# Performance work log

Hardware: AMD Instinct MI355X
Metric: run time of the kernel (lower is better)

The kernel has to match this reference:

```python
import jax, jax.numpy as jnp
import numpy as np

DIM = 512; HEADS = 8; KVH = 2; DH = 64; SEG = 1024; EPS = 1e-12
NA = 4096; NX = 4096; B = 2


def _mh_rmsnorm(t, gamma):
    # t: [b,h,n,d]; F.normalize (L2 with eps clamp) * gamma * sqrt(d)
    norm = jnp.maximum(jnp.linalg.norm(t, axis=-1, keepdims=True), EPS)
    return (t / norm) * gamma * (DH ** 0.5)


def _rope(t, pos):
    # rotate-half RoPE over full head dim
    half = DH // 2
    inv_freq = 1.0 / (10000.0 ** (jnp.arange(half, dtype=jnp.float32) / half))
    freqs = pos[:, None] * inv_freq[None, :]            # [n, half]
    cos = jnp.concatenate([jnp.cos(freqs)] * 2, -1)     # [n, d]
    sin = jnp.concatenate([jnp.sin(freqs)] * 2, -1)
    t1, t2 = jnp.split(t, 2, axis=-1)
    rot = jnp.concatenate([-t2, t1], -1)
    return t * cos + rot * sin


def _attend(q, k, v, beta):
    # infini-attention: per-segment causal softmax + kernelized recurrent memory
    b, h, n, d = q.shape
    pos = jnp.arange(n, dtype=jnp.float32)
    q = _rope(q, pos)
    k = _rope(k, pos)
    scale = d ** -0.5
    ns = n // SEG
    seg = lambda t: t.reshape(b, h, ns, SEG, d).transpose(2, 0, 1, 3, 4)
    qs, ks, vs = seg(q), seg(k), seg(v)                 # [ns,b,h,SEG,d]
    causal = jnp.tril(jnp.ones((SEG, SEG), dtype=bool))
    gate = jax.nn.sigmoid(beta)[None, :, None, None]    # [1,h,1,1]

    def step(carry, inp):
        M, z = carry                                    # [b,h,d,d], [b,h,d]
        qi, ki, vi = inp
        sq = jax.nn.elu(qi) + 1.0
        sk = jax.nn.elu(ki) + 1.0
        mem_num = jnp.einsum('bhnd,bhde->bhne', sq, M)
        mem_den = jnp.einsum('bhnd,bhd->bhn', sq, z)[..., None] + EPS
        a_mem = mem_num / mem_den
        scores = jnp.einsum('bhnd,bhmd->bhnm', qi, ki) * scale
        scores = jnp.where(causal, scores, -jnp.inf)
        a_loc = jnp.einsum('bhnm,bhmd->bhnd', jax.nn.softmax(scores, -1), vi)
        out = gate * a_mem + (1.0 - gate) * a_loc
        M = M + jnp.einsum('bhnd,bhne->bhde', sk, vi)
        z = z + sk.sum(axis=2)
        return (M, z), out

    M0 = jnp.zeros((b, h, d, d), q.dtype)
    z0 = jnp.zeros((b, h, d), q.dtype)
    _, outs = jax.lax.scan(step, (M0, z0), (qs, ks, vs))  # [ns,b,h,SEG,d]
    return outs.transpose(1, 2, 0, 3, 4).reshape(b, h, n, d)


def _heads(t, h):
    b, n, hd = t.shape
    return t.reshape(b, n, h, hd // h).transpose(0, 2, 1, 3)


def setup_inputs() -> dict:
    key = jax.random.key(0)
    ks = jax.random.split(key, 16)
    d = {}
    d['x'] = jax.random.normal(ks[0], (B, NX, DIM), jnp.float32)
    d['a'] = jax.random.normal(ks[1], (B, NA, DIM), jnp.float32)
    scale = 1.0 / np.sqrt(DIM)
    proj = [('Wq_x', HEADS * DH), ('Wk_x', KVH * DH), ('Wv_x', KVH * DH),
            ('Wq_a', HEADS * DH), ('Wk_a', KVH * DH), ('Wv_a', KVH * DH)]
    for i, (name, cout) in enumerate(proj):
        d[name] = jax.random.normal(ks[2 + i], (DIM, cout), jnp.float32) * scale
    d['gq_x'] = jnp.ones((HEADS, 1, DH), jnp.float32)
    d['gk_x'] = jnp.ones((KVH, 1, DH), jnp.float32)
    d['gq_a'] = jnp.ones((HEADS, 1, DH), jnp.float32)
    d['gk_a'] = jnp.ones((KVH, 1, DH), jnp.float32)
    d['beta'] = jnp.zeros((HEADS,), jnp.float32)
    return d


def reference(x, a, Wq_x, Wk_x, Wv_x, Wq_a, Wk_a, Wv_a, gq_x, gk_x, gq_a, gk_a, beta):
    rep = HEADS // KVH
    q_x = _mh_rmsnorm(_heads(x @ Wq_x, HEADS), gq_x)
    k_x = _mh_rmsnorm(_heads(x @ Wk_x, KVH), gk_x)
    v_x = _heads(x @ Wv_x, KVH)
    q_a = _mh_rmsnorm(_heads(a @ Wq_a, HEADS), gq_a)
    k_a = _mh_rmsnorm(_heads(a @ Wk_a, KVH), gk_a)
    v_a = _heads(a @ Wv_a, KVH)
    gqa = lambda t: jnp.tile(t, (1, rep, 1, 1))          # 'b h n d -> b (r h) n d'
    q = jnp.concatenate([q_a, q_x], axis=2)              # pack [a, x] along seq
    k = jnp.concatenate([gqa(k_a), gqa(k_x)], axis=2)
    v = jnp.concatenate([gqa(v_a), gqa(v_x)], axis=2)
    out = _attend(q, k, v, beta)
    out_a, out_x = out[:, :, :NA], out[:, :, NA:]
    merge = lambda t: t.transpose(0, 2, 1, 3).reshape(t.shape[0], t.shape[2], -1)
    return merge(out_x), merge(out_a)
```

## Files before the change

### kernel.cpp

```cpp
#include <hip/hip_runtime.h>
#include <math.h>

#define NH 8
#define NKV 2
#define SEGL 1024
#define NSEG 8
#define NTOK 8192
#define BATCH 2
#define DIMK 512

typedef short short8v __attribute__((ext_vector_type(8)));
typedef short short4v __attribute__((ext_vector_type(4)));
typedef float f32x4 __attribute__((ext_vector_type(4)));
typedef int int4v __attribute__((ext_vector_type(4)));

__device__ __forceinline__ unsigned short f2bf(float f) {
  union { float f; unsigned u; } c; c.f = f;
  unsigned u = c.u;
  return (unsigned short)((u + 0x7FFFu + ((u >> 16) & 1u)) >> 16);
}
__device__ __forceinline__ float bf2f(unsigned short h) {
  union { unsigned u; float f; } c; c.u = ((unsigned)h) << 16;
  return c.f;
}
__device__ __forceinline__ unsigned cvtpk(float lo, float hi) {
  unsigned r;
  asm("v_cvt_pk_bf16_f32 %0, %1, %2" : "=v"(r) : "v"(lo), "v"(hi));
  return r;
}

__device__ __forceinline__ void gload16(const unsigned short* g, unsigned short* l) {
  __builtin_amdgcn_global_load_lds(
      (const __attribute__((address_space(1))) unsigned int*)g,
      (__attribute__((address_space(3))) unsigned int*)l, 16, 0, 0);
}

__global__ void cast_bf16_kernel(const float* __restrict__ a, const float* __restrict__ x,
                                 unsigned short* __restrict__ outa,
                                 unsigned short* __restrict__ outx) {
  const float* in = blockIdx.y ? x : a;
  unsigned short* out = blockIdx.y ? outx : outa;
  int i = blockIdx.x * blockDim.x + threadIdx.x;
  const float4* p = (const float4*)in + (size_t)i * 2;
  float4 v0 = p[0], v1 = p[1];
  short8v o;
  o[0] = (short)f2bf(v0.x); o[1] = (short)f2bf(v0.y);
  o[2] = (short)f2bf(v0.z); o[3] = (short)f2bf(v0.w);
  o[4] = (short)f2bf(v1.x); o[5] = (short)f2bf(v1.y);
  o[6] = (short)f2bf(v1.z); o[7] = (short)f2bf(v1.w);
  *((short8v*)out + i) = o;
}

__global__ void rope_tab_kernel(float* __restrict__ tab) {
  const int i = blockIdx.x * 256 + threadIdx.x;
  const int pos = i >> 5, j = i & 31;
  const float LOG1E4 = 9.210340371976184f;
  float inv = __expf(-((float)j / 32.f) * LOG1E4);
  float sn, cs;
  sincosf((float)pos * inv, &sn, &cs);
  tab[(size_t)pos * 64 + j] = cs;
  tab[(size_t)pos * 64 + 32 + j] = sn;
}

__global__ void wtrans_kernel(const float* __restrict__ w0, const float* __restrict__ w1,
                              const float* __restrict__ w2, const float* __restrict__ w3,
                              const float* __restrict__ w4, const float* __restrict__ w5,
                              unsigned short* __restrict__ o0, unsigned short* __restrict__ o1,
                              unsigned short* __restrict__ o2, unsigned short* __restrict__ o3,
                              unsigned short* __restrict__ o4, unsigned short* __restrict__ o5) {
  __shared__ float T[32][33];
  const int z = blockIdx.z;
  const float* in; unsigned short* out; int C;
  switch (z) {
    case 0: in = w0; out = o0; C = 512; break;
    case 1: in = w1; out = o1; C = 128; break;
    case 2: in = w2; out = o2; C = 128; break;
    case 3: in = w3; out = o3; C = 512; break;
    case 4: in = w4; out = o4; C = 128; break;
    default: in = w5; out = o5; C = 128; break;
  }
  const int c0 = blockIdx.x * 32, k0 = blockIdx.y * 32;
  if (c0 >= C) return;
  const int tx = threadIdx.x & 31, ty = threadIdx.x >> 5;
  #pragma unroll
  for (int i = 0; i < 4; i++)
    T[ty + i * 8][tx] = in[(size_t)(k0 + ty + i * 8) * C + c0 + tx];
  __syncthreads();
  #pragma unroll
  for (int i = 0; i < 4; i++)
    out[(size_t)(c0 + ty + i * 8) * 512 + k0 + tx] = f2bf(T[tx][ty + i * 8]);
}

__global__ __launch_bounds__(256, 3) void proj_all_kernel(
    const unsigned short* __restrict__ Xa, const unsigned short* __restrict__ Xx,
    const unsigned short* __restrict__ WtQa, const unsigned short* __restrict__ WtKa,
    const unsigned short* __restrict__ WtVa, const unsigned short* __restrict__ WtQx,
    const unsigned short* __restrict__ WtKx, const unsigned short* __restrict__ WtVx,
    const float* __restrict__ gq_a, const float* __restrict__ gk_a,
    const float* __restrict__ gq_x, const float* __restrict__ gk_x,
    const float* __restrict__ Rtab,
    unsigned short* __restrict__ Qb, unsigned short* __restrict__ Kb,
    unsigned short* __restrict__ Kt, unsigned short* __restrict__ Vt)
{
  __shared__ __attribute__((aligned(16))) unsigned short Xs[2][128][64];
  __shared__ __attribute__((aligned(16))) unsigned short Ws2[2][64][64];
  unsigned short (*Tsh)[72] = (unsigned short (*)[72])&Xs[0][0][0];

  const int tid = threadIdx.x;
  const int w = tid >> 6, l = tid & 63, lc = l & 15, lg = l >> 4;
  const int r7 = lc & 7;
  const int z = blockIdx.z;
  const int y = blockIdx.y;
  const int row0 = blockIdx.x * 128;
  const int pos_offset = z ? 4096 : 0;

  const unsigned short* Xbf = z ? Xx : Xa;
  const unsigned short* Wt;
  const float* gamma = nullptr;
  unsigned short* OUT = nullptr;
  unsigned short* OUTT = nullptr;
  int h, Hout, doNR;
  if (y < 8) {
    h = y; Hout = NH; doNR = 1;
    Wt = z ? WtQx : WtQa; gamma = z ? gq_x : gq_a; OUT = Qb;
  } else if (y < 10) {
    h = y - 8; Hout = NKV; doNR = 1;
    Wt = z ? WtKx : WtKa; gamma = z ? gk_x : gk_a; OUT = Kb; OUTT = Kt;
  } else {
    h = y - 10; Hout = NKV; doNR = 0;
    Wt = z ? WtVx : WtVa; OUTT = Vt;
  }

  const int srow = tid >> 3;
  const int sg   = (tid & 7) ^ (srow & 7);
  const unsigned short* Xrow = Xbf + (size_t)(row0 + srow) * 512 + sg * 8;
  const unsigned short* Wrow = Wt + (size_t)(h * 64 + srow) * 512 + sg * 8;

  f32x4 acc[2][4];
  #pragma unroll
  for (int m = 0; m < 2; m++)
    #pragma unroll
    for (int ct = 0; ct < 4; ct++) { acc[m][ct][0]=0.f; acc[m][ct][1]=0.f; acc[m][ct][2]=0.f; acc[m][ct][3]=0.f; }

  #pragma unroll
  for (int p = 0; p < 4; p++)
    gload16(Xrow + (size_t)p * 32 * 512, &Xs[0][0][0] + p * 2048 + tid * 8);
  #pragma unroll
  for (int p = 0; p < 2; p++)
    gload16(Wrow + (size_t)p * 32 * 512, &Ws2[0][0][0] + p * 2048 + tid * 8);
  __syncthreads();

  for (int s = 0; s < 8; s++) {
    const int buf = s & 1;
    if (s < 7) {
      const int k0n = (s + 1) * 64;
      #pragma unroll
      for (int p = 0; p < 4; p++)
        gload16(Xrow + (size_t)p * 32 * 512 + k0n, &Xs[buf ^ 1][0][0] + p * 2048 + tid * 8);
      #pragma unroll
      for (int p = 0; p < 2; p++)
        gload16(Wrow + (size_t)p * 32 * 512 + k0n, &Ws2[buf ^ 1][0][0] + p * 2048 + tid * 8);
    }

    __builtin_amdgcn_s_setprio(1);
    #pragma unroll
    for (int kc = 0; kc < 2; kc++) {
      const int gsw = (((kc * 4 + lg) ^ r7) & 7) * 8;
      short8v a8[2], b8[4];
      #pragma unroll
      for (int m = 0; m < 2; m++)
        a8[m] = *(const short8v*)&Xs[buf][m * 64 + w * 16 + lc][gsw];
      #pragma unroll
      for (int ct = 0; ct < 4; ct++)
        b8[ct] = *(const short8v*)&Ws2[buf][ct * 16 + lc][gsw];
      #pragma unroll
      for (int m = 0; m < 2; m++)
        #pragma unroll
        for (int ct = 0; ct < 4; ct++)
          acc[m][ct] = __builtin_amdgcn_mfma_f32_16x16x32_bf16(a8[m], b8[ct], acc[m][ct], 0, 0, 0);
    }
    __builtin_amdgcn_s_setprio(0);
    __syncthreads();
  }

  float gam[4];
  if (doNR) {
    #pragma unroll
    for (int ct = 0; ct < 4; ct++) gam[ct] = gamma[h * 64 + ct * 16 + lc];
  }

  #pragma unroll
  for (int m = 0; m < 2; m++) {
    if (doNR) {
      float srw[4];
      #pragma unroll
      for (int reg = 0; reg < 4; reg++) {
        float ss = acc[m][0][reg]*acc[m][0][reg] + acc[m][1][reg]*acc[m][1][reg]
                 + acc[m][2][reg]*acc[m][2][reg] + acc[m][3][reg]*acc[m][3][reg];
        ss += __shfl_xor(ss, 1, 64);
        ss += __shfl_xor(ss, 2, 64);
        ss += __shfl_xor(ss, 4, 64);
        ss += __shfl_xor(ss, 8, 64);
        srw[reg] = 8.0f / fmaxf(sqrtf(ss), 1e-12f);
      }
      const int posb = pos_offset + ((row0 + m * 64) & 4095) + w * 16 + lg * 4;
      #pragma unroll
      for (int reg = 0; reg < 4; reg++) {
        const float* tabr = Rtab + (size_t)(posb + reg) * 64;
        #pragma unroll
        for (int half = 0; half < 2; half++) {
          float cs = tabr[half * 16 + lc];
          float sn = tabr[32 + half * 16 + lc];
          float v1 = acc[m][half][reg] * srw[reg] * gam[half];
          float v2 = acc[m][half + 2][reg] * srw[reg] * gam[half + 2];
          acc[m][half][reg]     = v1 * cs - v2 * sn;
          acc[m][half + 2][reg] = v2 * cs + v1 * sn;
        }
      }
    }

    #pragma unroll
    for (int ct = 0; ct < 4; ct++)
      #pragma unroll
      for (int reg = 0; reg < 4; reg++)
        Tsh[w * 16 + lg * 4 + reg][ct * 16 + lc] = f2bf(acc[m][ct][reg]);
    __syncthreads();

    const int growm = row0 + m * 64;
    const int b = growm >> 12;
    const int pos0 = pos_offset + (growm & 4095);
    if (OUT) {
      const int r = tid >> 2, part = tid & 3;
      unsigned short* dst = OUT + (((size_t)b * Hout + h) * NTOK + pos0 + r) * 64 + part * 16;
      short8v u0 = *(const short8v*)&Tsh[r][part * 16];
      short8v u1 = *(const short8v*)&Tsh[r][part * 16 + 8];
      *(short8v*)dst = u0;
      *(short8v*)(dst + 8) = u1;
    }
    if (OUTT) {
      const int e = tid >> 2, part = tid & 3;
      short8v t0, t1;
      #pragma unroll
      for (int jj = 0; jj < 16; jj++) {
        const int LG = ((part & 1) << 1) | (jj >> 3);
        const int H  = (jj >> 2) & 1;
        const int I  = jj & 3;
        const int srcrow = (part >> 1) * 32 + H * 16 + LG * 4 + I;
        unsigned short v = Tsh[srcrow][e];
        if (jj < 8) t0[jj] = (short)v; else t1[jj - 8] = (short)v;
      }
      unsigned short* dstT = OUTT + (((size_t)b * NKV + h) * 64 + e) * NTOK + pos0 + part * 16;
      *(short8v*)dstT = t0;
      *(short8v*)(dstT + 8) = t1;
    }
    __syncthreads();
  }
}

__global__ __launch_bounds__(256) void seg_summary_kernel(
    const unsigned short* __restrict__ Kt, const unsigned short* __restrict__ Vt,
    float* __restrict__ Spart, float* __restrict__ Zpart)
{
  const int blk = blockIdx.x;
  const int chunk = blk & 7;
  const int seg = (blk >> 3) & 7;
  const int bkv = blk >> 6;
  const int tid = threadIdx.x;
  const int w = tid >> 6, l = tid & 63, lc = l & 15, lg = l >> 4;
  const unsigned short* KtB = Kt + ((size_t)bkv * 64) * NTOK + seg * SEGL + chunk * 128;
  const unsigned short* VtB = Vt + ((size_t)bkv * 64) * NTOK + seg * SEGL + chunk * 128;

  f32x4 acc[4];
  #pragma unroll
  for (int ct = 0; ct < 4; ct++) { acc[ct][0]=0.f; acc[ct][1]=0.f; acc[ct][2]=0.f; acc[ct][3]=0.f; }
  float zacc[4] = {0.f, 0.f, 0.f, 0.f};

  for (int n0 = 0; n0 < 128; n0 += 32) {
    short8v av = *(const short8v*)(VtB + (size_t)(w * 16 + lc) * NTOK + n0 + lg * 8);
    #pragma unroll
    for (int ct = 0; ct < 4; ct++) {
      short8v kv = *(const short8v*)(KtB + (size_t)(ct * 16 + lc) * NTOK + n0 + lg * 8);
      short8v skv;
      float zp = 0.f;
      #pragma unroll
      for (int i = 0; i < 8; i++) {
        float kf = bf2f((unsigned short)kv[i]);
        float sk = kf > 0.f ? kf + 1.f : __expf(kf);
        zp += sk;
        skv[i] = (short)f2bf(sk);
      }
      zacc[ct] += zp;
      acc[ct] = __builtin_amdgcn_mfma_f32_16x16x32_bf16(av, skv, acc[ct], 0, 0, 0);
    }
  }

  float* Sp = Spart + (size_t)blk * 4096;
  #pragma unroll
  for (int ct = 0; ct < 4; ct++)
    #pragma unroll
    for (int reg = 0; reg < 4; reg++)
      Sp[(size_t)(w * 16 + lg * 4 + reg) * 64 + ct * 16 + lc] = acc[ct][reg];

  if (w == 0) {
    #pragma unroll
    for (int ct = 0; ct < 4; ct++) {
      zacc[ct] += __shfl_xor(zacc[ct], 16, 64);
      zacc[ct] += __shfl_xor(zacc[ct], 32, 64);
    }
    if (lg == 0) {
      float* Zp = Zpart + (size_t)blk * 64;
      #pragma unroll
      for (int ct = 0; ct < 4; ct++) Zp[ct * 16 + lc] = zacc[ct];
    }
  }
}

__global__ void prefix_kernel(const float* __restrict__ Spart, const float* __restrict__ Zpart,
                              unsigned short* __restrict__ PT, float* __restrict__ PZ)
{
  const int bkv = blockIdx.x;
  const int col = blockIdx.y * 256 + threadIdx.x;
  float run = 0.f;
  for (int s = 0; s < NSEG; s++) {
    float v = 0.f;
    #pragma unroll
    for (int c = 0; c < 8; c++)
      v += Spart[(((size_t)(bkv * 8 + s)) * 8 + c) * 4096 + col];
    PT[((size_t)bkv * 8 + s) * 4096 + col] = f2bf(run);
    run += v;
  }
  if (blockIdx.y == 0 && threadIdx.x < 64) {
    const int d = threadIdx.x;
    float rz = 0.f;
    for (int s = 0; s < NSEG; s++) {
      float v = 0.f;
      #pragma unroll
      for (int c = 0; c < 8; c++)
        v += Zpart[(((size_t)(bkv * 8 + s)) * 8 + c) * 64 + d];
      PZ[((size_t)bkv * 8 + s) * 64 + d] = rz;
      rz += v;
    }
  }
}

__global__ __launch_bounds__(256, 2) void attn_mfma_kernel(
    const unsigned short* __restrict__ Qb, const unsigned short* __restrict__ Kb,
    const unsigned short* __restrict__ Vt, const unsigned short* __restrict__ PT,
    const float* __restrict__ PZ, const float* __restrict__ beta,
    float* __restrict__ OUT)
{
  __shared__ __attribute__((aligned(16))) unsigned short Ks[2][64][64];
  __shared__ __attribute__((aligned(16))) unsigned short Vs[2][64][64];
  const int tid = threadIdx.x;
  const int w = tid >> 6;
  const int l = tid & 63;
  const int lc = l & 15;
  const int lg = l >> 4;
  const int r7 = lc & 7;

  const int bid = (blockIdx.x & 7) * 64 + (blockIdx.x >> 3);
  const int j   = bid & 7;
  const int seg = (bid >> 3) & 7;
  const int pp  = (bid >> 6) & 1;
  const int kv  = (bid >> 7) & 1;
  const int b   = bid >> 8;
  const int bkv = b * NKV + kv;
  const int qtA = 15 - j, qtB = j;
  const int segbase = seg * SEGL;

  const unsigned short* Kbase = Kb + ((size_t)bkv * NTOK + segbase) * 64;
  const unsigned short* Vbase = Vt + ((size_t)bkv * 64) * NTOK + segbase;

  const int srow = tid >> 3;
  const int sg   = (tid & 7) ^ (srow & 7);

  short8v aq0[2][2], aq1[2][2];
  #pragma unroll
  for (int hh = 0; hh < 2; hh++) {
    const int h = kv + 4 * pp + 2 * hh;
    const int bh = b * NH + h;
    {
      const unsigned short* qp =
          Qb + (((size_t)bh * NTOK) + segbase + qtA * 64 + w * 16 + lc) * 64 + lg * 8;
      aq0[hh][0] = *(const short8v*)(qp);
      aq1[hh][0] = *(const short8v*)(qp + 32);
    }
    {
      const unsigned short* qp =
          Qb + (((size_t)bh * NTOK) + segbase + qtB * 64 + w * 16 + lc) * 64 + lg * 8;
      aq0[hh][1] = *(const short8v*)(qp);
      aq1[hh][1] = *(const short8v*)(qp + 32);
    }
  }

  f32x4 O[2][2][4];
  #pragma unroll
  for (int hh = 0; hh < 2; hh++)
    #pragma unroll
    for (int tt = 0; tt < 2; tt++)
      #pragma unroll
      for (int ce = 0; ce < 4; ce++) { O[hh][tt][ce][0]=0.f; O[hh][tt][ce][1]=0.f; O[hh][tt][ce][2]=0.f; O[hh][tt][ce][3]=0.f; }
  float rsumL[2][2] = {{0.f, 0.f}, {0.f, 0.f}};

  const float c1 = 0.125f * 1.44269504089f;
  const float c2 = 8.0f * 1.44269504089f;

  {
    unsigned short* kD = &Ks[0][0][0];
    unsigned short* vD = &Vs[0][0][0];
    #pragma unroll
    for (int p = 0; p < 2; p++) {
      const int row = p * 32 + srow;
      gload16(Kbase + (size_t)row * 64 + sg * 8, kD + p * 2048 + tid * 8);
      gload16(Vbase + (size_t)row * NTOK + sg * 8, vD + p * 2048 + tid * 8);
    }
  }
  __syncthreads();

  for (int kt = 0; kt <= qtA; ++kt) {
    const int buf = kt & 1;
    if (kt < qtA) {
      const int ktn = kt + 1;
      unsigned short* kD = &Ks[buf ^ 1][0][0];
      unsigned short* vD = &Vs[buf ^ 1][0][0];
      #pragma unroll
      for (int p = 0; p < 2; p++) {
        const int row = p * 32 + srow;
        gload16(Kbase + (size_t)(ktn * 64 + row) * 64 + sg * 8, kD + p * 2048 + tid * 8);
        gload16(Vbase + (size_t)row * NTOK + ktn * 64 + sg * 8, vD + p * 2048 + tid * 8);
      }
    }

    __builtin_amdgcn_s_setprio(1);

    short8v ak0r[4], ak1r[4];
    #pragma unroll
    for (int ck = 0; ck < 4; ck++) {
      const int krow = ck * 16 + lc;
      ak0r[ck] = *(const short8v*)&Ks[buf][krow][((lg ^ r7) & 7) * 8];
      ak1r[ck] = *(const short8v*)&Ks[buf][krow][(((lg + 4) ^ r7) & 7) * 8];
    }
    short8v bvr[2][4];
    #pragma unroll
    for (int cp = 0; cp < 2; cp++)
      #pragma unroll
      for (int ce = 0; ce < 4; ce++)
        bvr[cp][ce] = *(const short8v*)&Vs[buf][ce * 16 + lc][(((cp * 4 + lg) ^ r7) & 7) * 8];

    #pragma unroll
    for (int hh = 0; hh < 2; hh++) {
      #pragma unroll
      for (int tt = 0; tt < 2; tt++) {
        if (tt == 1 && kt > qtB) continue;
        const int qt_ = tt ? qtB : qtA;
        const bool diag = (kt == qt_);
        const int ctmax = diag ? w : 3;

        unsigned paw[4][2];
        #pragma unroll
        for (int ck = 0; ck < 4; ck++) {
          if (ck > ctmax) { paw[ck][0] = 0u; paw[ck][1] = 0u; continue; }
          f32x4 s;
          s[0]=0.f; s[1]=0.f; s[2]=0.f; s[3]=0.f;
          s = __builtin_amdgcn_mfma_f32_16x16x32_bf16(ak0r[ck], aq0[hh][tt], s, 0, 0, 0);
          s = __builtin_amdgcn_mfma_f32_16x16x32_bf16(ak1r[ck], aq1[hh][tt], s, 0, 0, 0);
          const bool needmask = diag && (ck == w);
          float p0 = exp2f(s[0] * c1 - c2);
          float p1 = exp2f(s[1] * c1 - c2);
          float p2 = exp2f(s[2] * c1 - c2);
          float p3 = exp2f(s[3] * c1 - c2);
          if (needmask) {
            if (lg * 4 + 0 > lc) p0 = 0.f;
            if (lg * 4 + 1 > lc) p1 = 0.f;
            if (lg * 4 + 2 > lc) p2 = 0.f;
            if (lg * 4 + 3 > lc) p3 = 0.f;
          }
          rsumL[hh][tt] += p0 + p1 + p2 + p3;
          paw[ck][0] = cvtpk(p0, p1);
          paw[ck][1] = cvtpk(p2, p3);
        }

        #pragma unroll
        for (int cp = 0; cp < 2; cp++) {
          if (cp * 2 > ctmax) continue;
          int4v a8i;
          a8i[0] = (int)paw[cp * 2][0];
          a8i[1] = (int)paw[cp * 2][1];
          a8i[2] = (int)paw[cp * 2 + 1][0];
          a8i[3] = (int)paw[cp * 2 + 1][1];
          short8v a8;
          __builtin_memcpy(&a8, &a8i, 16);
          #pragma unroll
          for (int ce = 0; ce < 4; ce++)
            O[hh][tt][ce] = __builtin_amdgcn_mfma_f32_16x16x32_bf16(a8, bvr[cp][ce], O[hh][tt][ce], 0, 0, 0);
        }
      }
    }
    __builtin_amdgcn_s_setprio(0);
    __syncthreads();
  }

  const unsigned short* stp = PT + ((size_t)bkv * NSEG + seg) * 4096 + lc * 64 + lg * 8;
  const float* zp = PZ + ((size_t)bkv * NSEG + seg) * 64 + lg * 8;

  #pragma unroll
  for (int hh = 0; hh < 2; hh++) {
    const int h = kv + 4 * pp + 2 * hh;
    const float g = 1.f / (1.f + __expf(-beta[h]));
    const float g1 = 1.f - g;

    #pragma unroll
    for (int tt = 0; tt < 2; tt++) {
      float rsum = rsumL[hh][tt];
      rsum += __shfl_xor(rsum, 16, 64);
      rsum += __shfl_xor(rsum, 32, 64);

      float sq0[8], sq1[8];
      float den = 1e-12f;
      #pragma unroll
      for (int i = 0; i < 8; i++) {
        float f0 = bf2f((unsigned short)aq0[hh][tt][i]);
        sq0[i] = f0 > 0.f ? f0 + 1.f : __expf(f0);
        den += sq0[i] * zp[i];
        float f1 = bf2f((unsigned short)aq1[hh][tt][i]);
        sq1[i] = f1 > 0.f ? f1 + 1.f : __expf(f1);
        den += sq1[i] * zp[32 + i];
      }
      int4v q0i, q1i;
      q0i[0] = (int)cvtpk(sq0[0], sq0[1]);
      q0i[1] = (int)cvtpk(sq0[2], sq0[3]);
      q0i[2] = (int)cvtpk(sq0[4], sq0[5]);
      q0i[3] = (int)cvtpk(sq0[6], sq0[7]);
      q1i[0] = (int)cvtpk(sq1[0], sq1[1]);
      q1i[1] = (int)cvtpk(sq1[2], sq1[3]);
      q1i[2] = (int)cvtpk(sq1[4], sq1[5]);
      q1i[3] = (int)cvtpk(sq1[6], sq1[7]);
      short8v asq0, asq1;
      __builtin_memcpy(&asq0, &q0i, 16);
      __builtin_memcpy(&asq1, &q1i, 16);

      f32x4 N[4];
      #pragma unroll
      for (int ct = 0; ct < 4; ct++) { N[ct][0]=0.f; N[ct][1]=0.f; N[ct][2]=0.f; N[ct][3]=0.f; }
      #pragma unroll
      for (int ct = 0; ct < 4; ct++) {
        short8v bs0 = *(const short8v*)(stp + ct * 16 * 64);
        short8v bs1 = *(const short8v*)(stp + ct * 16 * 64 + 32);
        N[ct] = __builtin_amdgcn_mfma_f32_16x16x32_bf16(asq0, bs0, N[ct], 0, 0, 0);
        N[ct] = __builtin_amdgcn_mfma_f32_16x16x32_bf16(asq1, bs1, N[ct], 0, 0, 0);
      }
      den += __shfl_xor(den, 16, 64);
      den += __shfl_xor(den, 32, 64);
      float denc[4], rs[4];
      #pragma unroll
      for (int reg = 0; reg < 4; reg++) {
        denc[reg] = __shfl(den, lg * 4 + reg, 64);
        rs[reg]   = __shfl(rsum, lg * 4 + reg, 64);
      }

      const int q0 = (tt ? qtB : qtA) * 64;
      const int nrow = segbase + q0 + w * 16 + lg * 4;
      #pragma unroll
      for (int reg = 0; reg < 4; reg++) {
        const int n = nrow + reg;
        const float invs = 1.f / rs[reg];
        const float invd = 1.f / denc[reg];
        size_t obase;
        if (n < 4096) obase = (size_t)BATCH * 4096 * 512 + (((size_t)b * 4096 + n) * NH + h) * 64;
        else          obase = (((size_t)b * 4096 + (n - 4096)) * NH + h) * 64;
        #pragma unroll
        for (int ce = 0; ce < 4; ce++) {
          OUT[obase + ce * 16 + lc] = g * N[ce][reg] * invd + g1 * O[hh][tt][ce][reg] * invs;
        }
      }
    }
  }
}

extern "C" void kernel_launch(void* const* d_in, const int* in_sizes, int n_in,
                              void* d_out, int out_size, void* d_ws, size_t ws_size,
                              hipStream_t stream) {
  const float* x    = (const float*)d_in[0];
  const float* a    = (const float*)d_in[1];
  const float* Wq_x = (const float*)d_in[2];
  const float* Wk_x = (const float*)d_in[3];
  const float* Wv_x = (const float*)d_in[4];
  const float* Wq_a = (const float*)d_in[5];
  const float* Wk_a = (const float*)d_in[6];
  const float* Wv_a = (const float*)d_in[7];
  const float* gq_x = (const float*)d_in[8];
  const float* gk_x = (const float*)d_in[9];
  const float* gq_a = (const float*)d_in[10];
  const float* gk_a = (const float*)d_in[11];
  const float* beta = (const float*)d_in[12];

  unsigned short* Qb = (unsigned short*)d_ws;
  unsigned short* Kb = Qb + (size_t)8388608;
  unsigned short* Kt = Kb + (size_t)2097152;
  unsigned short* Vt = Kt + (size_t)2097152;
  unsigned short* Xa = Vt + (size_t)2097152;
  unsigned short* Xx = Xa + (size_t)4194304;
  unsigned short* WtQa = Xx + (size_t)4194304;
  unsigned short* WtKa = WtQa + (size_t)262144;
  unsigned short* WtVa = WtKa + (size_t)65536;
  unsigned short* WtQx = WtVa + (size_t)65536;
  unsigned short* WtKx = WtQx + (size_t)262144;
  unsigned short* WtVx = WtKx + (size_t)65536;
  float* Spart = (float*)(WtVx + (size_t)65536);
  float* Zpart = Spart + (size_t)1048576;
  float* PZ = Zpart + (size_t)16384;
  unsigned short* PT = (unsigned short*)(PZ + (size_t)2048);
  float* Rtab = (float*)(PT + (size_t)131072);

  cast_bf16_kernel<<<dim3(2048, 2), 256, 0, stream>>>(a, x, Xa, Xx);
  rope_tab_kernel<<<1024, 256, 0, stream>>>(Rtab);
  wtrans_kernel<<<dim3(16, 16, 6), 256, 0, stream>>>(
      Wq_a, Wk_a, Wv_a, Wq_x, Wk_x, Wv_x, WtQa, WtKa, WtVa, WtQx, WtKx, WtVx);
  proj_all_kernel<<<dim3(64, 12, 2), 256, 0, stream>>>(
      Xa, Xx, WtQa, WtKa, WtVa, WtQx, WtKx, WtVx,
      gq_a, gk_a, gq_x, gk_x, Rtab, Qb, Kb, Kt, Vt);
  seg_summary_kernel<<<256, 256, 0, stream>>>(Kt, Vt, Spart, Zpart);
  prefix_kernel<<<dim3(4, 16), 256, 0, stream>>>(Spart, Zpart, PT, PZ);
  attn_mfma_kernel<<<dim3(512), 256, 0, stream>>>(Qb, Kb, Vt, PT, PZ, beta, (float*)d_out);
}
```

Before: 93.80 us.

## Split attention blocks to one head each and fuse rope table into wtrans

The attention kernel now processes one query head per block instead of two, doubling the grid to 1024 blocks and raising the launch-bounds occupancy hint from 2 to 4 blocks per CU. This cuts per-thread registers and adds parallelism, at the cost of loading each K/V tile into shared memory twice as often. Separately, the RoPE table computation is folded into the weight-transpose kernel as an extra z-slice, removing one kernel launch.

```diff
diff --git a/kernel.cpp b/kernel.cpp
--- a/kernel.cpp
+++ b/kernel.cpp
@@ -51,25 +51,30 @@
   *((short8v*)out + i) = o;
 }
 
-__global__ void rope_tab_kernel(float* __restrict__ tab) {
-  const int i = blockIdx.x * 256 + threadIdx.x;
-  const int pos = i >> 5, j = i & 31;
-  const float LOG1E4 = 9.210340371976184f;
-  float inv = __expf(-((float)j / 32.f) * LOG1E4);
-  float sn, cs;
-  sincosf((float)pos * inv, &sn, &cs);
-  tab[(size_t)pos * 64 + j] = cs;
-  tab[(size_t)pos * 64 + 32 + j] = sn;
-}
-
 __global__ void wtrans_kernel(const float* __restrict__ w0, const float* __restrict__ w1,
                               const float* __restrict__ w2, const float* __restrict__ w3,
                               const float* __restrict__ w4, const float* __restrict__ w5,
                               unsigned short* __restrict__ o0, unsigned short* __restrict__ o1,
                               unsigned short* __restrict__ o2, unsigned short* __restrict__ o3,
-                              unsigned short* __restrict__ o4, unsigned short* __restrict__ o5) {
+                              unsigned short* __restrict__ o4, unsigned short* __restrict__ o5,
+                              float* __restrict__ rtab) {
   __shared__ float T[32][33];
   const int z = blockIdx.z;
+  if (z == 6) {
+    const int flat = blockIdx.y * 16 + blockIdx.x;
+    const int base = (flat * 256 + threadIdx.x) * 8;
+    const float LOG1E4 = 9.210340371976184f;
+    #pragma unroll
+    for (int k = 0; k < 8; k++) {
+      int e = base + k;
+      int pos = e >> 6, c = e & 63, jj = c & 31;
+      float inv = __expf(-((float)jj / 32.f) * LOG1E4);
+      float sn, cs;
+      sincosf((float)pos * inv, &sn, &cs);
+      rtab[e] = (c < 32) ? cs : sn;
+    }
+    return;
+  }
   const float* in; unsigned short* out; int C;
   switch (z) {
     case 0: in = w0; out = o0; C = 512; break;
@@ -343,7 +348,7 @@
   }
 }
 
-__global__ __launch_bounds__(256, 2) void attn_mfma_kernel(
+__global__ __launch_bounds__(256, 4) void attn_mfma_kernel(
     const unsigned short* __restrict__ Qb, const unsigned short* __restrict__ Kb,
     const unsigned short* __restrict__ Vt, const unsigned short* __restrict__ PT,
     const float* __restrict__ PZ, const float* __restrict__ beta,
@@ -358,12 +363,14 @@
   const int lg = l >> 4;
   const int r7 = lc & 7;
 
-  const int bid = (blockIdx.x & 7) * 64 + (blockIdx.x >> 3);
+  const int bid = (blockIdx.x & 7) * 128 + (blockIdx.x >> 3);
   const int j   = bid & 7;
   const int seg = (bid >> 3) & 7;
-  const int pp  = (bid >> 6) & 1;
-  const int kv  = (bid >> 7) & 1;
-  const int b   = bid >> 8;
+  const int hi  = (bid >> 6) & 3;
+  const int kv  = (bid >> 8) & 1;
+  const int b   = bid >> 9;
+  const int h   = kv + 2 * hi;
+  const int bh  = b * NH + h;
   const int bkv = b * NKV + kv;
   const int qtA = 15 - j, qtB = j;
   const int segbase = seg * SEGL;
@@ -374,33 +381,26 @@
   const int srow = tid >> 3;
   const int sg   = (tid & 7) ^ (srow & 7);
 
-  short8v aq0[2][2], aq1[2][2];
-  #pragma unroll
-  for (int hh = 0; hh < 2; hh++) {
-    const int h = kv + 4 * pp + 2 * hh;
-    const int bh = b * NH + h;
-    {
-      const unsigned short* qp =
-          Qb + (((size_t)bh * NTOK) + segbase + qtA * 64 + w * 16 + lc) * 64 + lg * 8;
-      aq0[hh][0] = *(const short8v*)(qp);
-      aq1[hh][0] = *(const short8v*)(qp + 32);
-    }
-    {
-      const unsigned short* qp =
-          Qb + (((size_t)bh * NTOK) + segbase + qtB * 64 + w * 16 + lc) * 64 + lg * 8;
-      aq0[hh][1] = *(const short8v*)(qp);
-      aq1[hh][1] = *(const short8v*)(qp + 32);
-    }
-  }
-
-  f32x4 O[2][2][4];
-  #pragma unroll
-  for (int hh = 0; hh < 2; hh++)
-    #pragma unroll
-    for (int tt = 0; tt < 2; tt++)
-      #pragma unroll
-      for (int ce = 0; ce < 4; ce++) { O[hh][tt][ce][0]=0.f; O[hh][tt][ce][1]=0.f; O[hh][tt][ce][2]=0.f; O[hh][tt][ce][3]=0.f; }
-  float rsumL[2][2] = {{0.f, 0.f}, {0.f, 0.f}};
+  short8v aq0[2], aq1[2];
+  {
+    const unsigned short* qp =
+        Qb + (((size_t)bh * NTOK) + segbase + qtA * 64 + w * 16 + lc) * 64 + lg * 8;
+    aq0[0] = *(const short8v*)(qp);
+    aq1[0] = *(const short8v*)(qp + 32);
+  }
+  {
+    const unsigned short* qp =
+        Qb + (((size_t)bh * NTOK) + segbase + qtB * 64 + w * 16 + lc) * 64 + lg * 8;
+    aq0[1] = *(const short8v*)(qp);
+    aq1[1] = *(const short8v*)(qp + 32);
+  }
+
+  f32x4 O[2][4];
+  #pragma unroll
+  for (int tt = 0; tt < 2; tt++)
+    #pragma unroll
+    for (int ce = 0; ce < 4; ce++) { O[tt][ce][0]=0.f; O[tt][ce][1]=0.f; O[tt][ce][2]=0.f; O[tt][ce][3]=0.f; }
+  float rsumL[2] = {0.f, 0.f};
 
   const float c1 = 0.125f * 1.44269504089f;
   const float c2 = 8.0f * 1.44269504089f;
@@ -448,52 +448,49 @@
         bvr[cp][ce] = *(const short8v*)&Vs[buf][ce * 16 + lc][(((cp * 4 + lg) ^ r7) & 7) * 8];
 
     #pragma unroll
-    for (int hh = 0; hh < 2; hh++) {
-      #pragma unroll
-      for (int tt = 0; tt < 2; tt++) {
-        if (tt == 1 && kt > qtB) continue;
-        const int qt_ = tt ? qtB : qtA;
-        const bool diag = (kt == qt_);
-        const int ctmax = diag ? w : 3;
-
-        unsigned paw[4][2];
+    for (int tt = 0; tt < 2; tt++) {
+      if (tt == 1 && kt > qtB) continue;
+      const int qt_ = tt ? qtB : qtA;
+      const bool diag = (kt == qt_);
+      const int ctmax = diag ? w : 3;
+
+      unsigned paw[4][2];
+      #pragma unroll
+      for (int ck = 0; ck < 4; ck++) {
+        if (ck > ctmax) { paw[ck][0] = 0u; paw[ck][1] = 0u; continue; }
+        f32x4 s;
+        s[0]=0.f; s[1]=0.f; s[2]=0.f; s[3]=0.f;
+        s = __builtin_amdgcn_mfma_f32_16x16x32_bf16(ak0r[ck], aq0[tt], s, 0, 0, 0);
+        s = __builtin_amdgcn_mfma_f32_16x16x32_bf16(ak1r[ck], aq1[tt], s, 0, 0, 0);
+        const bool needmask = diag && (ck == w);
+        float p0 = exp2f(s[0] * c1 - c2);
+        float p1 = exp2f(s[1] * c1 - c2);
+        float p2 = exp2f(s[2] * c1 - c2);
+        float p3 = exp2f(s[3] * c1 - c2);
+        if (needmask) {
+          if (lg * 4 + 0 > lc) p0 = 0.f;
+          if (lg * 4 + 1 > lc) p1 = 0.f;
+          if (lg * 4 + 2 > lc) p2 = 0.f;
+          if (lg * 4 + 3 > lc) p3 = 0.f;
+        }
+        rsumL[tt] += p0 + p1 + p2 + p3;
+        paw[ck][0] = cvtpk(p0, p1);
+        paw[ck][1] = cvtpk(p2, p3);
+      }
+
+      #pragma unroll
+      for (int cp = 0; cp < 2; cp++) {
+        if (cp * 2 > ctmax) continue;
+        int4v a8i;
+        a8i[0] = (int)paw[cp * 2][0];
+        a8i[1] = (int)paw[cp * 2][1];
+        a8i[2] = (int)paw[cp * 2 + 1][0];
+        a8i[3] = (int)paw[cp * 2 + 1][1];
+        short8v a8;
+        __builtin_memcpy(&a8, &a8i, 16);
         #pragma unroll
-        for (int ck = 0; ck < 4; ck++) {
-          if (ck > ctmax) { paw[ck][0] = 0u; paw[ck][1] = 0u; continue; }
-          f32x4 s;
-          s[0]=0.f; s[1]=0.f; s[2]=0.f; s[3]=0.f;
-          s = __builtin_amdgcn_mfma_f32_16x16x32_bf16(ak0r[ck], aq0[hh][tt], s, 0, 0, 0);
-          s = __builtin_amdgcn_mfma_f32_16x16x32_bf16(ak1r[ck], aq1[hh][tt], s, 0, 0, 0);
-          const bool needmask = diag && (ck == w);
-          float p0 = exp2f(s[0] * c1 - c2);
-          float p1 = exp2f(s[1] * c1 - c2);
-          float p2 = exp2f(s[2] * c1 - c2);
-          float p3 = exp2f(s[3] * c1 - c2);
-          if (needmask) {
-            if (lg * 4 + 0 > lc) p0 = 0.f;
-            if (lg * 4 + 1 > lc) p1 = 0.f;
-            if (lg * 4 + 2 > lc) p2 = 0.f;
-            if (lg * 4 + 3 > lc) p3 = 0.f;
-          }
-          rsumL[hh][tt] += p0 + p1 + p2 + p3;
-          paw[ck][0] = cvtpk(p0, p1);
-          paw[ck][1] = cvtpk(p2, p3);
-        }
-
-        #pragma unroll
-        for (int cp = 0; cp < 2; cp++) {
-          if (cp * 2 > ctmax) continue;
-          int4v a8i;
-          a8i[0] = (int)paw[cp * 2][0];
-          a8i[1] = (int)paw[cp * 2][1];
-          a8i[2] = (int)paw[cp * 2 + 1][0];
-          a8i[3] = (int)paw[cp * 2 + 1][1];
-          short8v a8;
-          __builtin_memcpy(&a8, &a8i, 16);
-          #pragma unroll
-          for (int ce = 0; ce < 4; ce++)
-            O[hh][tt][ce] = __builtin_amdgcn_mfma_f32_16x16x32_bf16(a8, bvr[cp][ce], O[hh][tt][ce], 0, 0, 0);
-        }
+        for (int ce = 0; ce < 4; ce++)
+          O[tt][ce] = __builtin_amdgcn_mfma_f32_16x16x32_bf16(a8, bvr[cp][ce], O[tt][ce], 0, 0, 0);
       }
     }
     __builtin_amdgcn_s_setprio(0);
@@ -502,76 +499,71 @@
 
   const unsigned short* stp = PT + ((size_t)bkv * NSEG + seg) * 4096 + lc * 64 + lg * 8;
   const float* zp = PZ + ((size_t)bkv * NSEG + seg) * 64 + lg * 8;
-
-  #pragma unroll
-  for (int hh = 0; hh < 2; hh++) {
-    const int h = kv + 4 * pp + 2 * hh;
-    const float g = 1.f / (1.f + __expf(-beta[h]));
-    const float g1 = 1.f - g;
-
-    #pragma unroll
-    for (int tt = 0; tt < 2; tt++) {
-      float rsum = rsumL[hh][tt];
-      rsum += __shfl_xor(rsum, 16, 64);
-      rsum += __shfl_xor(rsum, 32, 64);
-
-      float sq0[8], sq1[8];
-      float den = 1e-12f;
-      #pragma unroll
-      for (int i = 0; i < 8; i++) {
-        float f0 = bf2f((unsigned short)aq0[hh][tt][i]);
-        sq0[i] = f0 > 0.f ? f0 + 1.f : __expf(f0);
-        den += sq0[i] * zp[i];
-        float f1 = bf2f((unsigned short)aq1[hh][tt][i]);
-        sq1[i] = f1 > 0.f ? f1 + 1.f : __expf(f1);
-        den += sq1[i] * zp[32 + i];
-      }
-      int4v q0i, q1i;
-      q0i[0] = (int)cvtpk(sq0[0], sq0[1]);
-      q0i[1] = (int)cvtpk(sq0[2], sq0[3]);
-      q0i[2] = (int)cvtpk(sq0[4], sq0[5]);
-      q0i[3] = (int)cvtpk(sq0[6], sq0[7]);
-      q1i[0] = (int)cvtpk(sq1[0], sq1[1]);
-      q1i[1] = (int)cvtpk(sq1[2], sq1[3]);
-      q1i[2] = (int)cvtpk(sq1[4], sq1[5]);
-      q1i[3] = (int)cvtpk(sq1[6], sq1[7]);
-      short8v asq0, asq1;
-      __builtin_memcpy(&asq0, &q0i, 16);
-      __builtin_memcpy(&asq1, &q1i, 16);
-
-      f32x4 N[4];
-      #pragma unroll
-      for (int ct = 0; ct < 4; ct++) { N[ct][0]=0.f; N[ct][1]=0.f; N[ct][2]=0.f; N[ct][3]=0.f; }
-      #pragma unroll
-      for (int ct = 0; ct < 4; ct++) {
-        short8v bs0 = *(const short8v*)(stp + ct * 16 * 64);
-        short8v bs1 = *(const short8v*)(stp + ct * 16 * 64 + 32);
-        N[ct] = __builtin_amdgcn_mfma_f32_16x16x32_bf16(asq0, bs0, N[ct], 0, 0, 0);
-        N[ct] = __builtin_amdgcn_mfma_f32_16x16x32_bf16(asq1, bs1, N[ct], 0, 0, 0);
-      }
-      den += __shfl_xor(den, 16, 64);
-      den += __shfl_xor(den, 32, 64);
-      float denc[4], rs[4];
-      #pragma unroll
-      for (int reg = 0; reg < 4; reg++) {
-        denc[reg] = __shfl(den, lg * 4 + reg, 64);
-        rs[reg]   = __shfl(rsum, lg * 4 + reg, 64);
-      }
-
-      const int q0 = (tt ? qtB : qtA) * 64;
-      const int nrow = segbase + q0 + w * 16 + lg * 4;
-      #pragma unroll
-      for (int reg = 0; reg < 4; reg++) {
-        const int n = nrow + reg;
-        const float invs = 1.f / rs[reg];
-        const float invd = 1.f / denc[reg];
-        size_t obase;
-        if (n < 4096) obase = (size_t)BATCH * 4096 * 512 + (((size_t)b * 4096 + n) * NH + h) * 64;
-        else          obase = (((size_t)b * 4096 + (n - 4096)) * NH + h) * 64;
-        #pragma unroll
-        for (int ce = 0; ce < 4; ce++) {
-          OUT[obase + ce * 16 + lc] = g * N[ce][reg] * invd + g1 * O[hh][tt][ce][reg] * invs;
-        }
+  const float g = 1.f / (1.f + __expf(-beta[h]));
+  const float g1 = 1.f - g;
+
+  #pragma unroll
+  for (int tt = 0; tt < 2; tt++) {
+    float rsum = rsumL[tt];
+    rsum += __shfl_xor(rsum, 16, 64);
+    rsum += __shfl_xor(rsum, 32, 64);
+
+    float sq0[8], sq1[8];
+    float den = 1e-12f;
+    #pragma unroll
+    for (int i = 0; i < 8; i++) {
+      float f0 = bf2f((unsigned short)aq0[tt][i]);
+      sq0[i] = f0 > 0.f ? f0 + 1.f : __expf(f0);
+      den += sq0[i] * zp[i];
+      float f1 = bf2f((unsigned short)aq1[tt][i]);
+      sq1[i] = f1 > 0.f ? f1 + 1.f : __expf(f1);
+      den += sq1[i] * zp[32 + i];
+    }
+    int4v q0i, q1i;
+    q0i[0] = (int)cvtpk(sq0[0], sq0[1]);
+    q0i[1] = (int)cvtpk(sq0[2], sq0[3]);
+    q0i[2] = (int)cvtpk(sq0[4], sq0[5]);
+    q0i[3] = (int)cvtpk(sq0[6], sq0[7]);
+    q1i[0] = (int)cvtpk(sq1[0], sq1[1]);
+    q1i[1] = (int)cvtpk(sq1[2], sq1[3]);
+    q1i[2] = (int)cvtpk(sq1[4], sq1[5]);
+    q1i[3] = (int)cvtpk(sq1[6], sq1[7]);
+    short8v asq0, asq1;
+    __builtin_memcpy(&asq0, &q0i, 16);
+    __builtin_memcpy(&asq1, &q1i, 16);
+
+    f32x4 N[4];
+    #pragma unroll
+    for (int ct = 0; ct < 4; ct++) { N[ct][0]=0.f; N[ct][1]=0.f; N[ct][2]=0.f; N[ct][3]=0.f; }
+    #pragma unroll
+    for (int ct = 0; ct < 4; ct++) {
+      short8v bs0 = *(const short8v*)(stp + ct * 16 * 64);
+      short8v bs1 = *(const short8v*)(stp + ct * 16 * 64 + 32);
+      N[ct] = __builtin_amdgcn_mfma_f32_16x16x32_bf16(asq0, bs0, N[ct], 0, 0, 0);
+      N[ct] = __builtin_amdgcn_mfma_f32_16x16x32_bf16(asq1, bs1, N[ct], 0, 0, 0);
+    }
+    den += __shfl_xor(den, 16, 64);
+    den += __shfl_xor(den, 32, 64);
+    float denc[4], rs[4];
+    #pragma unroll
+    for (int reg = 0; reg < 4; reg++) {
+      denc[reg] = __shfl(den, lg * 4 + reg, 64);
+      rs[reg]   = __shfl(rsum, lg * 4 + reg, 64);
+    }
+
+    const int q0 = (tt ? qtB : qtA) * 64;
+    const int nrow = segbase + q0 + w * 16 + lg * 4;
+    #pragma unroll
+    for (int reg = 0; reg < 4; reg++) {
+      const int n = nrow + reg;
+      const float invs = 1.f / rs[reg];
+      const float invd = 1.f / denc[reg];
+      size_t obase;
+      if (n < 4096) obase = (size_t)BATCH * 4096 * 512 + (((size_t)b * 4096 + n) * NH + h) * 64;
+      else          obase = (((size_t)b * 4096 + (n - 4096)) * NH + h) * 64;
+      #pragma unroll
+      for (int ce = 0; ce < 4; ce++) {
+        OUT[obase + ce * 16 + lc] = g * N[ce][reg] * invd + g1 * O[tt][ce][reg] * invs;
       }
     }
   }
@@ -613,13 +605,12 @@
   float* Rtab = (float*)(PT + (size_t)131072);
 
   cast_bf16_kernel<<<dim3(2048, 2), 256, 0, stream>>>(a, x, Xa, Xx);
-  rope_tab_kernel<<<1024, 256, 0, stream>>>(Rtab);
-  wtrans_kernel<<<dim3(16, 16, 6), 256, 0, stream>>>(
-      Wq_a, Wk_a, Wv_a, Wq_x, Wk_x, Wv_x, WtQa, WtKa, WtVa, WtQx, WtKx, WtVx);
+  wtrans_kernel<<<dim3(16, 16, 7), 256, 0, stream>>>(
+      Wq_a, Wk_a, Wv_a, Wq_x, Wk_x, Wv_x, WtQa, WtKa, WtVa, WtQx, WtKx, WtVx, Rtab);
   proj_all_kernel<<<dim3(64, 12, 2), 256, 0, stream>>>(
       Xa, Xx, WtQa, WtKa, WtVa, WtQx, WtKx, WtVx,
       gq_a, gk_a, gq_x, gk_x, Rtab, Qb, Kb, Kt, Vt);
   seg_summary_kernel<<<256, 256, 0, stream>>>(Kt, Vt, Spart, Zpart);
   prefix_kernel<<<dim3(4, 16), 256, 0, stream>>>(Spart, Zpart, PT, PZ);
-  attn_mfma_kernel<<<dim3(512), 256, 0, stream>>>(Qb, Kb, Vt, PT, PZ, beta, (float*)d_out);
-}
+  attn_mfma_kernel<<<dim3(1024), 256, 0, stream>>>(Qb, Kb, Vt, PT, PZ, beta, (float*)d_out);
+}
```

After: 150.5 us. +60.4%, slower.

## Stage two KV tiles per barrier in attention and fold rope table into wtrans

Applied to the files above, without the earlier changes.

The attention kernel moves from a 2-deep to a 4-deep LDS ring and processes two key/value tiles between each barrier, prefetching the next two tiles while computing. This halves the number of __syncthreads per block and gives loads more time to land. Separately, the RoPE table generation is merged into the weight-transpose launch as an extra z-slice, which removes one kernel launch. LDS use per block doubles, which could limit occupancy at two blocks per CU, and the code size grows from duplicating the tile compute.

```diff
diff --git a/kernel.cpp b/kernel.cpp
--- a/kernel.cpp
+++ b/kernel.cpp
@@ -13,6 +13,8 @@
 typedef short short4v __attribute__((ext_vector_type(4)));
 typedef float f32x4 __attribute__((ext_vector_type(4)));
 typedef int int4v __attribute__((ext_vector_type(4)));
+
+#define MFMA16 __builtin_amdgcn_mfma_f32_16x16x32_bf16
 
 __device__ __forceinline__ unsigned short f2bf(float f) {
   union { float f; unsigned u; } c; c.f = f;
@@ -51,25 +53,30 @@
   *((short8v*)out + i) = o;
 }
 
-__global__ void rope_tab_kernel(float* __restrict__ tab) {
-  const int i = blockIdx.x * 256 + threadIdx.x;
-  const int pos = i >> 5, j = i & 31;
-  const float LOG1E4 = 9.210340371976184f;
-  float inv = __expf(-((float)j / 32.f) * LOG1E4);
-  float sn, cs;
-  sincosf((float)pos * inv, &sn, &cs);
-  tab[(size_t)pos * 64 + j] = cs;
-  tab[(size_t)pos * 64 + 32 + j] = sn;
-}
-
 __global__ void wtrans_kernel(const float* __restrict__ w0, const float* __restrict__ w1,
                               const float* __restrict__ w2, const float* __restrict__ w3,
                               const float* __restrict__ w4, const float* __restrict__ w5,
                               unsigned short* __restrict__ o0, unsigned short* __restrict__ o1,
                               unsigned short* __restrict__ o2, unsigned short* __restrict__ o3,
-                              unsigned short* __restrict__ o4, unsigned short* __restrict__ o5) {
+                              unsigned short* __restrict__ o4, unsigned short* __restrict__ o5,
+                              float* __restrict__ rtab) {
   __shared__ float T[32][33];
   const int z = blockIdx.z;
+  if (z == 6) {
+    const int flat = blockIdx.y * 16 + blockIdx.x;
+    const int base = (flat * 256 + threadIdx.x) * 8;
+    const float LOG1E4 = 9.210340371976184f;
+    #pragma unroll
+    for (int k = 0; k < 8; k++) {
+      int e = base + k;
+      int pos = e >> 6, c = e & 63, jj = c & 31;
+      float inv = __expf(-((float)jj / 32.f) * LOG1E4);
+      float sn, cs;
+      sincosf((float)pos * inv, &sn, &cs);
+      rtab[e] = (c < 32) ? cs : sn;
+    }
+    return;
+  }
   const float* in; unsigned short* out; int C;
   switch (z) {
     case 0: in = w0; out = o0; C = 512; break;
@@ -177,7 +184,7 @@
       for (int m = 0; m < 2; m++)
         #pragma unroll
         for (int ct = 0; ct < 4; ct++)
-          acc[m][ct] = __builtin_amdgcn_mfma_f32_16x16x32_bf16(a8[m], b8[ct], acc[m][ct], 0, 0, 0);
+          acc[m][ct] = MFMA16(a8[m], b8[ct], acc[m][ct], 0, 0, 0);
     }
     __builtin_amdgcn_s_setprio(0);
     __syncthreads();
@@ -290,7 +297,7 @@
         skv[i] = (short)f2bf(sk);
       }
       zacc[ct] += zp;
-      acc[ct] = __builtin_amdgcn_mfma_f32_16x16x32_bf16(av, skv, acc[ct], 0, 0, 0);
+      acc[ct] = MFMA16(av, skv, acc[ct], 0, 0, 0);
     }
   }
 
@@ -343,14 +350,95 @@
   }
 }
 
+#define STAGE_TILE(TILE, BUFN)                                                 \
+  do {                                                                         \
+    unsigned short* kD_ = &Ks[BUFN][0][0];                                     \
+    unsigned short* vD_ = &Vs[BUFN][0][0];                                     \
+    _Pragma("unroll")                                                          \
+    for (int p_ = 0; p_ < 2; p_++) {                                           \
+      const int row_ = p_ * 32 + srow;                                         \
+      gload16(Kbase + (size_t)((TILE) * 64 + row_) * 64 + sg * 8,              \
+              kD_ + p_ * 2048 + tid * 8);                                      \
+      gload16(Vbase + (size_t)row_ * NTOK + (TILE) * 64 + sg * 8,              \
+              vD_ + p_ * 2048 + tid * 8);                                      \
+    }                                                                          \
+  } while (0)
+
+#define COMPUTE_KT(KT)                                                         \
+  do {                                                                         \
+    const int kt_ = (KT);                                                      \
+    const int buf_ = kt_ & 3;                                                  \
+    short8v ak0r[4], ak1r[4];                                                  \
+    _Pragma("unroll")                                                          \
+    for (int ck = 0; ck < 4; ck++) {                                           \
+      const int krow = ck * 16 + lc;                                           \
+      ak0r[ck] = *(const short8v*)&Ks[buf_][krow][((lg ^ r7) & 7) * 8];        \
+      ak1r[ck] = *(const short8v*)&Ks[buf_][krow][(((lg + 4) ^ r7) & 7) * 8];  \
+    }                                                                          \
+    short8v bvr[2][4];                                                         \
+    _Pragma("unroll")                                                          \
+    for (int cp = 0; cp < 2; cp++)                                             \
+      _Pragma("unroll")                                                        \
+      for (int ce = 0; ce < 4; ce++)                                           \
+        bvr[cp][ce] =                                                          \
+            *(const short8v*)&Vs[buf_][ce * 16 + lc][(((cp * 4 + lg) ^ r7) & 7) * 8]; \
+    _Pragma("unroll")                                                          \
+    for (int hh = 0; hh < 2; hh++) {                                           \
+      _Pragma("unroll")                                                        \
+      for (int tt = 0; tt < 2; tt++) {                                         \
+        if (tt == 1 && kt_ > qtB) continue;                                    \
+        const int qt_ = tt ? qtB : qtA;                                        \
+        const bool diag = (kt_ == qt_);                                        \
+        const int ctmax = diag ? w : 3;                                        \
+        unsigned paw[4][2];                                                    \
+        _Pragma("unroll")                                                      \
+        for (int ck = 0; ck < 4; ck++) {                                       \
+          if (ck > ctmax) { paw[ck][0] = 0u; paw[ck][1] = 0u; continue; }      \
+          f32x4 s;                                                             \
+          s[0] = 0.f; s[1] = 0.f; s[2] = 0.f; s[3] = 0.f;                      \
+          s = MFMA16(ak0r[ck], aq0[hh][tt], s, 0, 0, 0);                       \
+          s = MFMA16(ak1r[ck], aq1[hh][tt], s, 0, 0, 0);                       \
+          const bool needmask = diag && (ck == w);                             \
+          float p0 = exp2f(s[0] * c1 - c2);                                    \
+          float p1 = exp2f(s[1] * c1 - c2);                                    \
+          float p2 = exp2f(s[2] * c1 - c2);                                    \
+          float p3 = exp2f(s[3] * c1 - c2);                                    \
+          if (needmask) {                                                      \
+            if (lg * 4 + 0 > lc) p0 = 0.f;                                     \
+            if (lg * 4 + 1 > lc) p1 = 0.f;                                     \
+            if (lg * 4 + 2 > lc) p2 = 0.f;                                     \
+            if (lg * 4 + 3 > lc) p3 = 0.f;                                     \
+          }                                                                    \
+          rsumL[hh][tt] += p0 + p1 + p2 + p3;                                  \
+          paw[ck][0] = cvtpk(p0, p1);                                          \
+          paw[ck][1] = cvtpk(p2, p3);                                          \
+        }                                                                      \
+        _Pragma("unroll")                                                      \
+        for (int cp = 0; cp < 2; cp++) {                                       \
+          if (cp * 2 > ctmax) continue;                                        \
+          int4v a8i;                                                           \
+          a8i[0] = (int)paw[cp * 2][0];                                        \
+          a8i[1] = (int)paw[cp * 2][1];                                        \
+          a8i[2] = (int)paw[cp * 2 + 1][0];                                    \
+          a8i[3] = (int)paw[cp * 2 + 1][1];                                    \
+          short8v a8;                                                          \
+          __builtin_memcpy(&a8, &a8i, 16);                                     \
+          _Pragma("unroll")                                                    \
+          for (int ce = 0; ce < 4; ce++)                                       \
+            O[hh][tt][ce] = MFMA16(a8, bvr[cp][ce], O[hh][tt][ce], 0, 0, 0);   \
+        }                                                                      \
+      }                                                                        \
+    }                                                                          \
+  } while (0)
+
 __global__ __launch_bounds__(256, 2) void attn_mfma_kernel(
     const unsigned short* __restrict__ Qb, const unsigned short* __restrict__ Kb,
     const unsigned short* __restrict__ Vt, const unsigned short* __restrict__ PT,
     const float* __restrict__ PZ, const float* __restrict__ beta,
     float* __restrict__ OUT)
 {
-  __shared__ __attribute__((aligned(16))) unsigned short Ks[2][64][64];
-  __shared__ __attribute__((aligned(16))) unsigned short Vs[2][64][64];
+  __shared__ __attribute__((aligned(16))) unsigned short Ks[4][64][64];
+  __shared__ __attribute__((aligned(16))) unsigned short Vs[4][64][64];
   const int tid = threadIdx.x;
   const int w = tid >> 6;
   const int l = tid & 63;
@@ -405,97 +493,17 @@
   const float c1 = 0.125f * 1.44269504089f;
   const float c2 = 8.0f * 1.44269504089f;
 
-  {
-    unsigned short* kD = &Ks[0][0][0];
-    unsigned short* vD = &Vs[0][0][0];
-    #pragma unroll
-    for (int p = 0; p < 2; p++) {
-      const int row = p * 32 + srow;
-      gload16(Kbase + (size_t)row * 64 + sg * 8, kD + p * 2048 + tid * 8);
-      gload16(Vbase + (size_t)row * NTOK + sg * 8, vD + p * 2048 + tid * 8);
-    }
-  }
+  STAGE_TILE(0, 0);
+  STAGE_TILE(1, 1);
   __syncthreads();
 
-  for (int kt = 0; kt <= qtA; ++kt) {
-    const int buf = kt & 1;
-    if (kt < qtA) {
-      const int ktn = kt + 1;
-      unsigned short* kD = &Ks[buf ^ 1][0][0];
-      unsigned short* vD = &Vs[buf ^ 1][0][0];
-      #pragma unroll
-      for (int p = 0; p < 2; p++) {
-        const int row = p * 32 + srow;
-        gload16(Kbase + (size_t)(ktn * 64 + row) * 64 + sg * 8, kD + p * 2048 + tid * 8);
-        gload16(Vbase + (size_t)row * NTOK + ktn * 64 + sg * 8, vD + p * 2048 + tid * 8);
-      }
-    }
+  for (int kt0 = 0; kt0 <= qtA; kt0 += 2) {
+    if (kt0 + 2 <= qtA) STAGE_TILE(kt0 + 2, (kt0 + 2) & 3);
+    if (kt0 + 3 <= qtA) STAGE_TILE(kt0 + 3, (kt0 + 3) & 3);
 
     __builtin_amdgcn_s_setprio(1);
-
-    short8v ak0r[4], ak1r[4];
-    #pragma unroll
-    for (int ck = 0; ck < 4; ck++) {
-      const int krow = ck * 16 + lc;
-      ak0r[ck] = *(const short8v*)&Ks[buf][krow][((lg ^ r7) & 7) * 8];
-      ak1r[ck] = *(const short8v*)&Ks[buf][krow][(((lg + 4) ^ r7) & 7) * 8];
-    }
-    short8v bvr[2][4];
-    #pragma unroll
-    for (int cp = 0; cp < 2; cp++)
-      #pragma unroll
-      for (int ce = 0; ce < 4; ce++)
-        bvr[cp][ce] = *(const short8v*)&Vs[buf][ce * 16 + lc][(((cp * 4 + lg) ^ r7) & 7) * 8];
-
-    #pragma unroll
-    for (int hh = 0; hh < 2; hh++) {
-      #pragma unroll
-      for (int tt = 0; tt < 2; tt++) {
-        if (tt == 1 && kt > qtB) continue;
-        const int qt_ = tt ? qtB : qtA;
-        const bool diag = (kt == qt_);
-        const int ctmax = diag ? w : 3;
-
-        unsigned paw[4][2];
-        #pragma unroll
-        for (int ck = 0; ck < 4; ck++) {
-          if (ck > ctmax) { paw[ck][0] = 0u; paw[ck][1] = 0u; continue; }
-          f32x4 s;
-          s[0]=0.f; s[1]=0.f; s[2]=0.f; s[3]=0.f;
-          s = __builtin_amdgcn_mfma_f32_16x16x32_bf16(ak0r[ck], aq0[hh][tt], s, 0, 0, 0);
-          s = __builtin_amdgcn_mfma_f32_16x16x32_bf16(ak1r[ck], aq1[hh][tt], s, 0, 0, 0);
-          const bool needmask = diag && (ck == w);
-          float p0 = exp2f(s[0] * c1 - c2);
-          float p1 = exp2f(s[1] * c1 - c2);
-          float p2 = exp2f(s[2] * c1 - c2);
-          float p3 = exp2f(s[3] * c1 - c2);
-          if (needmask) {
-            if (lg * 4 + 0 > lc) p0 = 0.f;
-            if (lg * 4 + 1 > lc) p1 = 0.f;
-            if (lg * 4 + 2 > lc) p2 = 0.f;
-            if (lg * 4 + 3 > lc) p3 = 0.f;
-          }
-          rsumL[hh][tt] += p0 + p1 + p2 + p3;
-          paw[ck][0] = cvtpk(p0, p1);
-          paw[ck][1] = cvtpk(p2, p3);
-        }
-
-        #pragma unroll
-        for (int cp = 0; cp < 2; cp++) {
-          if (cp * 2 > ctmax) continue;
-          int4v a8i;
-          a8i[0] = (int)paw[cp * 2][0];
-          a8i[1] = (int)paw[cp * 2][1];
-          a8i[2] = (int)paw[cp * 2 + 1][0];
-          a8i[3] = (int)paw[cp * 2 + 1][1];
-          short8v a8;
-          __builtin_memcpy(&a8, &a8i, 16);
-          #pragma unroll
-          for (int ce = 0; ce < 4; ce++)
-            O[hh][tt][ce] = __builtin_amdgcn_mfma_f32_16x16x32_bf16(a8, bvr[cp][ce], O[hh][tt][ce], 0, 0, 0);
-        }
-      }
-    }
+    COMPUTE_KT(kt0);
+    if (kt0 + 1 <= qtA) COMPUTE_KT(kt0 + 1);
     __builtin_amdgcn_s_setprio(0);
     __syncthreads();
   }
@@ -546,8 +554,8 @@
       for (int ct = 0; ct < 4; ct++) {
         short8v bs0 = *(const short8v*)(stp + ct * 16 * 64);
         short8v bs1 = *(const short8v*)(stp + ct * 16 * 64 + 32);
-        N[ct] = __builtin_amdgcn_mfma_f32_16x16x32_bf16(asq0, bs0, N[ct], 0, 0, 0);
-        N[ct] = __builtin_amdgcn_mfma_f32_16x16x32_bf16(asq1, bs1, N[ct], 0, 0, 0);
+        N[ct] = MFMA16(asq0, bs0, N[ct], 0, 0, 0);
+        N[ct] = MFMA16(asq1, bs1, N[ct], 0, 0, 0);
       }
       den += __shfl_xor(den, 16, 64);
       den += __shfl_xor(den, 32, 64);
@@ -613,9 +621,8 @@
   float* Rtab = (float*)(PT + (size_t)131072);
 
   cast_bf16_kernel<<<dim3(2048, 2), 256, 0, stream>>>(a, x, Xa, Xx);
-  rope_tab_kernel<<<1024, 256, 0, stream>>>(Rtab);
-  wtrans_kernel<<<dim3(16, 16, 6), 256, 0, stream>>>(
-      Wq_a, Wk_a, Wv_a, Wq_x, Wk_x, Wv_x, WtQa, WtKa, WtVa, WtQx, WtKx, WtVx);
+  wtrans_kernel<<<dim3(16, 16, 7), 256, 0, stream>>>(
+      Wq_a, Wk_a, Wv_a, Wq_x, Wk_x, Wv_x, WtQa, WtKa, WtVa, WtQx, WtKx, WtVx, Rtab);
   proj_all_kernel<<<dim3(64, 12, 2), 256, 0, stream>>>(
       Xa, Xx, WtQa, WtKa, WtVa, WtQx, WtKx, WtVx,
       gq_a, gk_a, gq_x, gk_x, Rtab, Qb, Kb, Kt, Vt);
```

Result: no change. 93.92 us (+0.1%).
